# Kernel tuning notes

Hardware: AMD Instinct MI355X
Metric: run time of the kernel (lower is better)

Reference implementation:

```python
import jax, jax.numpy as jnp
import numpy as np

NCODEBOOKS, K, SUBVEC = 32, 16, 128
IN_F, OUT_F = 4096, 2048
BATCH, SEQ = 2, 1024


def setup_inputs() -> dict:
    key = jax.random.key(0)
    k1, k2, k3, k4, k5 = jax.random.split(key, 5)
    return {
        "x": jax.random.normal(k1, (BATCH, SEQ, IN_F), dtype=jnp.float32),
        "centroids": jax.random.normal(k2, (NCODEBOOKS, K, SUBVEC), dtype=jnp.float32),
        "weight": jax.random.normal(k3, (NCODEBOOKS, SUBVEC, OUT_F), dtype=jnp.float32),
        "inverse_temperature_logit": jax.random.normal(k4, (1,), dtype=jnp.float32),
        "bias": jax.random.normal(k5, (OUT_F,), dtype=jnp.float32),
    }


def reference(x, centroids, weight, inverse_temperature_logit, bias):
    shape = x.shape[:-1]
    C, k, d = centroids.shape
    # [N, C, d] -> [C, N, d]
    xr = jnp.transpose(x.reshape(-1, C, d), (1, 0, 2))
    # Euclidean cdist per codebook: [C, N, k]
    x2 = jnp.sum(xr * xr, axis=-1)[:, :, None]
    c2 = jnp.sum(centroids * centroids, axis=-1)[:, None, :]
    xc = jnp.einsum('cnd,ckd->cnk', xr, centroids)
    dist = jnp.sqrt(jnp.maximum(x2 + c2 - 2.0 * xc, 0.0))
    inv_temp = jax.nn.softplus(inverse_temperature_logit) + 1.0  # [1]
    attention = jax.nn.softmax(-dist * inv_temp, axis=-1)  # [C, N, k]
    lut = jnp.einsum('ckd,cdo->cko', centroids, weight)  # [C, k, O]
    training_output = jnp.einsum('cnk,cko->no', attention, lut)  # [N, O]
    # one-hot argmin matmul == direct gather of lut rows
    idx = jnp.argmin(dist, axis=-1)  # [C, N]
    gathered = jnp.take_along_axis(lut, idx[:, :, None], axis=1)  # [C, N, O]
    inference_output = jnp.sum(gathered, axis=0)  # [N, O]
    # straight-through estimator
    output = training_output - jax.lax.stop_gradient(training_output - inference_output)
    output = output + bias
    return output.reshape(*shape, lut.shape[-1])
```

## Files before the change

### kernel.cpp

```cpp
#include <hip/hip_runtime.h>

#define NCB 32
#define KK 16
#define DD 128
#define IN_F 4096
#define OUT_F 2048
#define NTOK 2048

__global__ __launch_bounds__(256) void lut_kernel(const float* __restrict__ centroids,
                                                  const float* __restrict__ weight,
                                                  float* __restrict__ lut,
                                                  float* __restrict__ c2out) {
    const int c = blockIdx.y;
    const int o0 = blockIdx.x * 64;
    const int lane_o = threadIdx.x & 63;
    const int dg = threadIdx.x >> 6;
    __shared__ float part[4][KK][64];

    if (blockIdx.x == 0 && threadIdx.x < KK) {
        const float* cb = centroids + ((size_t)c * KK + threadIdx.x) * DD;
        float s = 0.f;
        for (int d = 0; d < DD; ++d) { float v = cb[d]; s += v * v; }
        c2out[c * KK + threadIdx.x] = s;
    }

    float acc[KK];
#pragma unroll
    for (int k = 0; k < KK; ++k) acc[k] = 0.f;
    const float* wbase = weight + (size_t)c * DD * OUT_F + o0 + lane_o;
    const float* cbase = centroids + (size_t)c * KK * DD;
#pragma unroll
    for (int chunk = 0; chunk < 8; ++chunk) {
        const int d = dg * 32 + chunk * 4;
        float w0 = wbase[(size_t)(d + 0) * OUT_F];
        float w1 = wbase[(size_t)(d + 1) * OUT_F];
        float w2 = wbase[(size_t)(d + 2) * OUT_F];
        float w3 = wbase[(size_t)(d + 3) * OUT_F];
#pragma unroll
        for (int k = 0; k < KK; ++k) {
            float4 cv = *(const float4*)(cbase + k * DD + d);
            acc[k] += cv.x * w0 + cv.y * w1 + cv.z * w2 + cv.w * w3;
        }
    }
#pragma unroll
    for (int k = 0; k < KK; ++k) part[dg][k][lane_o] = acc[k];
    __syncthreads();
#pragma unroll
    for (int r = 0; r < 4; ++r) {
        int i = r * 256 + threadIdx.x;
        int k = i >> 6, o = i & 63;
        float s = part[0][k][o] + part[1][k][o] + part[2][k][o] + part[3][k][o];
        lut[((size_t)c * KK + k) * OUT_F + o0 + o] = s;
    }
}

__global__ __launch_bounds__(256) void idx_kernel(const float* __restrict__ x,
                                                  const float* __restrict__ centroids,
                                                  const float* __restrict__ c2,
                                                  unsigned char* __restrict__ idxb) {
    const int c = blockIdx.y;
    const int t0 = blockIdx.x * 64;
    const int tid = threadIdx.x;
    const int th_q = tid & 3;
    const int th_k = (tid >> 2) & 3;
    const int th_t = tid >> 4;

    __shared__ float cent_s[KK * 164];

    for (int p = tid; p < KK * 32; p += 256) {
        int k = p >> 5, f4 = p & 31;
        int q = f4 >> 3, jj = f4 & 7;
        *(float4*)(cent_s + k * 164 + q * 40 + jj * 4) =
            *(const float4*)(centroids + ((size_t)c * KK + k) * DD + f4 * 4);
    }
    __syncthreads();

    float c2v[4];
#pragma unroll
    for (int kk = 0; kk < 4; ++kk) c2v[kk] = c2[c * KK + th_k * 4 + kk];

    float acc[4][4];
#pragma unroll
    for (int r = 0; r < 4; ++r)
#pragma unroll
        for (int kk = 0; kk < 4; ++kk) acc[r][kk] = 0.f;

    const float* xb0 = x + (size_t)(t0 + th_t * 4) * IN_F + c * DD + th_q * 32;
#pragma unroll
    for (int chunk = 0; chunk < 8; ++chunk) {
        float4 xa[4];
#pragma unroll
        for (int r = 0; r < 4; ++r)
            xa[r] = *(const float4*)(xb0 + (size_t)r * IN_F + chunk * 4);
        float4 ca[4];
#pragma unroll
        for (int kk = 0; kk < 4; ++kk)
            ca[kk] = *(const float4*)(cent_s + (th_k * 4 + kk) * 164 + th_q * 40 + chunk * 4);
#pragma unroll
        for (int r = 0; r < 4; ++r)
#pragma unroll
            for (int kk = 0; kk < 4; ++kk)
                acc[r][kk] += xa[r].x * ca[kk].x + xa[r].y * ca[kk].y
                            + xa[r].z * ca[kk].z + xa[r].w * ca[kk].w;
    }

#pragma unroll
    for (int r = 0; r < 4; ++r)
#pragma unroll
        for (int kk = 0; kk < 4; ++kk) {
            float a = acc[r][kk];
            a += __shfl_xor(a, 1);
            a += __shfl_xor(a, 2);
            acc[r][kk] = a;
        }

#pragma unroll
    for (int r = 0; r < 4; ++r) {
        float best = c2v[0] - 2.f * acc[r][0];
        int bi = th_k * 4;
#pragma unroll
        for (int kk = 1; kk < 4; ++kk) {
            float v = c2v[kk] - 2.f * acc[r][kk];
            if (v < best) { best = v; bi = th_k * 4 + kk; }
        }
#pragma unroll
        for (int s = 4; s <= 8; s <<= 1) {
            float ov = __shfl_xor(best, s);
            int oi = __shfl_xor(bi, s);
            if (ov < best || (ov == best && oi < bi)) { best = ov; bi = oi; }
        }
        if ((tid & 15) == 0)
            idxb[(size_t)(t0 + th_t * 4 + r) * NCB + c] = (unsigned char)bi;
    }
}

__global__ __launch_bounds__(256) void gather_kernel(const float* __restrict__ lut,
                                                     const unsigned char* __restrict__ idxb,
                                                     const float* __restrict__ bias,
                                                     float* __restrict__ out) {
    const int t0 = blockIdx.x * 256;
    const int o0 = blockIdx.y * 32;
    __shared__ float slut[NCB * KK * 36];
    __shared__ unsigned char sidx[256 * NCB];

    {
        const int row = threadIdx.x >> 3;
        const int q = threadIdx.x & 7;
        for (int r = row; r < NCB * KK; r += 32)
            *(float4*)(slut + r * 36 + q * 4) =
                *(const float4*)(lut + (size_t)r * OUT_F + o0 + q * 4);
    }
    {
        const int4* ig = (const int4*)(idxb + (size_t)t0 * NCB);
        int4* is4 = (int4*)sidx;
        for (int i = threadIdx.x; i < 512; i += 256) is4[i] = ig[i];
    }
    __syncthreads();

    const int oo = (threadIdx.x & 15) * 2;
    const int tl = threadIdx.x >> 4;
    const float2 bv = *(const float2*)(bias + o0 + oo);

    for (int tt = tl; tt < 256; tt += 16) {
        float2 acc = bv;
        const unsigned int* ip = (const unsigned int*)(sidx + tt * NCB);
#pragma unroll
        for (int c4 = 0; c4 < NCB / 4; ++c4) {
            unsigned int iv4 = ip[c4];
#pragma unroll
            for (int b = 0; b < 4; ++b) {
                int cc = c4 * 4 + b;
                int iv = (iv4 >> (8 * b)) & 0xff;
                const float2 v = *(const float2*)(slut + (cc * KK + iv) * 36 + oo);
                acc.x += v.x;
                acc.y += v.y;
            }
        }
        *(float2*)(out + (size_t)(t0 + tt) * OUT_F + o0 + oo) = acc;
    }
}

extern "C" void kernel_launch(void* const* d_in, const int* in_sizes, int n_in,
                              void* d_out, int out_size, void* d_ws, size_t ws_size,
                              hipStream_t stream) {
    const float* x         = (const float*)d_in[0];
    const float* centroids = (const float*)d_in[1];
    const float* weight    = (const float*)d_in[2];
    const float* bias      = (const float*)d_in[4];
    float* out = (float*)d_out;

    float* lut = (float*)d_ws;
    unsigned char* idxb = (unsigned char*)d_ws + (4u << 20);
    float* c2 = (float*)((char*)d_ws + (4u << 20) + (64u << 10));

    lut_kernel<<<dim3(OUT_F / 64, NCB), 256, 0, stream>>>(centroids, weight, lut, c2);
    idx_kernel<<<dim3(NTOK / 64, NCB), 256, 0, stream>>>(x, centroids, c2, idxb);
    gather_kernel<<<dim3(NTOK / 256, OUT_F / 32), 256, 0, stream>>>(lut, idxb, bias, out);
}
```

Before: 163.1 us.

## Fuse LUT and index kernels into one launch with in-kernel centroid norms

Merges the LUT matmul kernel and the nearest-centroid index kernel into one launch, with block ID ranges picking the role. The index blocks now compute centroid squared norms from shared memory themselves, which removes the c2 dependency between the two former kernels. This saves one launch and lets the two independent workloads run concurrently on the GPU. The cost is extra redundant norm FLOPs in every index block and 16KB dynamic shared memory for all blocks, which may reduce occupancy.

```diff
diff --git a/kernel.cpp b/kernel.cpp
--- a/kernel.cpp
+++ b/kernel.cpp
@@ -6,131 +6,132 @@
 #define IN_F 4096
 #define OUT_F 2048
 #define NTOK 2048
+#define LUT_BLOCKS ((OUT_F / 64) * NCB)
+#define IDX_BLOCKS ((NTOK / 64) * NCB)
 
-__global__ __launch_bounds__(256) void lut_kernel(const float* __restrict__ centroids,
-                                                  const float* __restrict__ weight,
-                                                  float* __restrict__ lut,
-                                                  float* __restrict__ c2out) {
-    const int c = blockIdx.y;
-    const int o0 = blockIdx.x * 64;
-    const int lane_o = threadIdx.x & 63;
-    const int dg = threadIdx.x >> 6;
-    __shared__ float part[4][KK][64];
+__global__ __launch_bounds__(256) void fused_lut_idx(
+    const float* __restrict__ centroids, const float* __restrict__ weight,
+    const float* __restrict__ x, float* __restrict__ lut,
+    unsigned char* __restrict__ idxb) {
+    extern __shared__ float smem[];
+    const int tid = threadIdx.x;
 
-    if (blockIdx.x == 0 && threadIdx.x < KK) {
-        const float* cb = centroids + ((size_t)c * KK + threadIdx.x) * DD;
-        float s = 0.f;
-        for (int d = 0; d < DD; ++d) { float v = cb[d]; s += v * v; }
-        c2out[c * KK + threadIdx.x] = s;
-    }
+    if (blockIdx.x < LUT_BLOCKS) {
+        const int c = blockIdx.x >> 5;
+        const int o0 = (blockIdx.x & 31) * 64;
+        const int lane_o = tid & 63;
+        const int dg = tid >> 6;
+        float acc[KK];
+#pragma unroll
+        for (int k = 0; k < KK; ++k) acc[k] = 0.f;
+        const float* wbase = weight + (size_t)c * DD * OUT_F + o0 + lane_o;
+        const float* cbase = centroids + (size_t)c * KK * DD;
+#pragma unroll
+        for (int chunk = 0; chunk < 8; ++chunk) {
+            const int d = dg * 32 + chunk * 4;
+            float w0 = wbase[(size_t)(d + 0) * OUT_F];
+            float w1 = wbase[(size_t)(d + 1) * OUT_F];
+            float w2 = wbase[(size_t)(d + 2) * OUT_F];
+            float w3 = wbase[(size_t)(d + 3) * OUT_F];
+#pragma unroll
+            for (int k = 0; k < KK; ++k) {
+                float4 cv = *(const float4*)(cbase + k * DD + d);
+                acc[k] += cv.x * w0 + cv.y * w1 + cv.z * w2 + cv.w * w3;
+            }
+        }
+        float* part = smem;
+#pragma unroll
+        for (int k = 0; k < KK; ++k) part[(dg * KK + k) * 64 + lane_o] = acc[k];
+        __syncthreads();
+#pragma unroll
+        for (int r = 0; r < 4; ++r) {
+            int i = r * 256 + tid;
+            int k = i >> 6, o = i & 63;
+            float s = part[(0 * KK + k) * 64 + o] + part[(1 * KK + k) * 64 + o]
+                    + part[(2 * KK + k) * 64 + o] + part[(3 * KK + k) * 64 + o];
+            lut[((size_t)c * KK + k) * OUT_F + o0 + o] = s;
+        }
+    } else {
+        const int bid = blockIdx.x - LUT_BLOCKS;
+        const int c = bid & (NCB - 1);
+        const int t0 = (bid >> 5) * 64;
+        float* cent_s = smem;
+        const int th_q = tid & 3;
+        const int th_k = (tid >> 2) & 3;
+        const int th_t = tid >> 4;
 
-    float acc[KK];
-#pragma unroll
-    for (int k = 0; k < KK; ++k) acc[k] = 0.f;
-    const float* wbase = weight + (size_t)c * DD * OUT_F + o0 + lane_o;
-    const float* cbase = centroids + (size_t)c * KK * DD;
-#pragma unroll
-    for (int chunk = 0; chunk < 8; ++chunk) {
-        const int d = dg * 32 + chunk * 4;
-        float w0 = wbase[(size_t)(d + 0) * OUT_F];
-        float w1 = wbase[(size_t)(d + 1) * OUT_F];
-        float w2 = wbase[(size_t)(d + 2) * OUT_F];
-        float w3 = wbase[(size_t)(d + 3) * OUT_F];
-#pragma unroll
-        for (int k = 0; k < KK; ++k) {
-            float4 cv = *(const float4*)(cbase + k * DD + d);
-            acc[k] += cv.x * w0 + cv.y * w1 + cv.z * w2 + cv.w * w3;
+        for (int p = tid; p < KK * 32; p += 256) {
+            int k = p >> 5, f4 = p & 31;
+            int q = f4 >> 3, jj = f4 & 7;
+            *(float4*)(cent_s + k * 164 + q * 40 + jj * 4) =
+                *(const float4*)(centroids + ((size_t)c * KK + k) * DD + f4 * 4);
         }
-    }
-#pragma unroll
-    for (int k = 0; k < KK; ++k) part[dg][k][lane_o] = acc[k];
-    __syncthreads();
-#pragma unroll
-    for (int r = 0; r < 4; ++r) {
-        int i = r * 256 + threadIdx.x;
-        int k = i >> 6, o = i & 63;
-        float s = part[0][k][o] + part[1][k][o] + part[2][k][o] + part[3][k][o];
-        lut[((size_t)c * KK + k) * OUT_F + o0 + o] = s;
-    }
-}
+        __syncthreads();
 
-__global__ __launch_bounds__(256) void idx_kernel(const float* __restrict__ x,
-                                                  const float* __restrict__ centroids,
-                                                  const float* __restrict__ c2,
-                                                  unsigned char* __restrict__ idxb) {
-    const int c = blockIdx.y;
-    const int t0 = blockIdx.x * 64;
-    const int tid = threadIdx.x;
-    const int th_q = tid & 3;
-    const int th_k = (tid >> 2) & 3;
-    const int th_t = tid >> 4;
-
-    __shared__ float cent_s[KK * 164];
-
-    for (int p = tid; p < KK * 32; p += 256) {
-        int k = p >> 5, f4 = p & 31;
-        int q = f4 >> 3, jj = f4 & 7;
-        *(float4*)(cent_s + k * 164 + q * 40 + jj * 4) =
-            *(const float4*)(centroids + ((size_t)c * KK + k) * DD + f4 * 4);
-    }
-    __syncthreads();
-
-    float c2v[4];
-#pragma unroll
-    for (int kk = 0; kk < 4; ++kk) c2v[kk] = c2[c * KK + th_k * 4 + kk];
-
-    float acc[4][4];
-#pragma unroll
-    for (int r = 0; r < 4; ++r)
-#pragma unroll
-        for (int kk = 0; kk < 4; ++kk) acc[r][kk] = 0.f;
-
-    const float* xb0 = x + (size_t)(t0 + th_t * 4) * IN_F + c * DD + th_q * 32;
-#pragma unroll
-    for (int chunk = 0; chunk < 8; ++chunk) {
-        float4 xa[4];
-#pragma unroll
-        for (int r = 0; r < 4; ++r)
-            xa[r] = *(const float4*)(xb0 + (size_t)r * IN_F + chunk * 4);
-        float4 ca[4];
-#pragma unroll
-        for (int kk = 0; kk < 4; ++kk)
-            ca[kk] = *(const float4*)(cent_s + (th_k * 4 + kk) * 164 + th_q * 40 + chunk * 4);
+        float acc[4][4], sq[4];
 #pragma unroll
         for (int r = 0; r < 4; ++r)
 #pragma unroll
+            for (int kk = 0; kk < 4; ++kk) acc[r][kk] = 0.f;
+#pragma unroll
+        for (int kk = 0; kk < 4; ++kk) sq[kk] = 0.f;
+
+        const float* xb0 = x + (size_t)(t0 + th_t * 4) * IN_F + c * DD + th_q * 32;
+#pragma unroll
+        for (int chunk = 0; chunk < 8; ++chunk) {
+            float4 xa[4];
+#pragma unroll
+            for (int r = 0; r < 4; ++r)
+                xa[r] = *(const float4*)(xb0 + (size_t)r * IN_F + chunk * 4);
+            float4 ca[4];
+#pragma unroll
             for (int kk = 0; kk < 4; ++kk)
-                acc[r][kk] += xa[r].x * ca[kk].x + xa[r].y * ca[kk].y
-                            + xa[r].z * ca[kk].z + xa[r].w * ca[kk].w;
-    }
-
+                ca[kk] = *(const float4*)(cent_s + (th_k * 4 + kk) * 164 + th_q * 40 + chunk * 4);
 #pragma unroll
-    for (int r = 0; r < 4; ++r)
+            for (int kk = 0; kk < 4; ++kk)
+                sq[kk] += ca[kk].x * ca[kk].x + ca[kk].y * ca[kk].y
+                        + ca[kk].z * ca[kk].z + ca[kk].w * ca[kk].w;
+#pragma unroll
+            for (int r = 0; r < 4; ++r)
+#pragma unroll
+                for (int kk = 0; kk < 4; ++kk)
+                    acc[r][kk] += xa[r].x * ca[kk].x + xa[r].y * ca[kk].y
+                                + xa[r].z * ca[kk].z + xa[r].w * ca[kk].w;
+        }
 #pragma unroll
         for (int kk = 0; kk < 4; ++kk) {
-            float a = acc[r][kk];
+            float a = sq[kk];
             a += __shfl_xor(a, 1);
             a += __shfl_xor(a, 2);
-            acc[r][kk] = a;
-        }
-
-#pragma unroll
-    for (int r = 0; r < 4; ++r) {
-        float best = c2v[0] - 2.f * acc[r][0];
-        int bi = th_k * 4;
-#pragma unroll
-        for (int kk = 1; kk < 4; ++kk) {
-            float v = c2v[kk] - 2.f * acc[r][kk];
-            if (v < best) { best = v; bi = th_k * 4 + kk; }
+            sq[kk] = a;
         }
 #pragma unroll
-        for (int s = 4; s <= 8; s <<= 1) {
-            float ov = __shfl_xor(best, s);
-            int oi = __shfl_xor(bi, s);
-            if (ov < best || (ov == best && oi < bi)) { best = ov; bi = oi; }
+        for (int r = 0; r < 4; ++r)
+#pragma unroll
+            for (int kk = 0; kk < 4; ++kk) {
+                float a = acc[r][kk];
+                a += __shfl_xor(a, 1);
+                a += __shfl_xor(a, 2);
+                acc[r][kk] = a;
+            }
+#pragma unroll
+        for (int r = 0; r < 4; ++r) {
+            float best = sq[0] - 2.f * acc[r][0];
+            int bi = th_k * 4;
+#pragma unroll
+            for (int kk = 1; kk < 4; ++kk) {
+                float v = sq[kk] - 2.f * acc[r][kk];
+                if (v < best) { best = v; bi = th_k * 4 + kk; }
+            }
+#pragma unroll
+            for (int s = 4; s <= 8; s <<= 1) {
+                float ov = __shfl_xor(best, s);
+                int oi = __shfl_xor(bi, s);
+                if (ov < best || (ov == best && oi < bi)) { best = ov; bi = oi; }
+            }
+            if ((tid & 15) == 0)
+                idxb[(size_t)(t0 + th_t * 4 + r) * NCB + c] = (unsigned char)bi;
         }
-        if ((tid & 15) == 0)
-            idxb[(size_t)(t0 + th_t * 4 + r) * NCB + c] = (unsigned char)bi;
     }
 }
 
@@ -191,9 +192,8 @@
 
     float* lut = (float*)d_ws;
     unsigned char* idxb = (unsigned char*)d_ws + (4u << 20);
-    float* c2 = (float*)((char*)d_ws + (4u << 20) + (64u << 10));
 
-    lut_kernel<<<dim3(OUT_F / 64, NCB), 256, 0, stream>>>(centroids, weight, lut, c2);
-    idx_kernel<<<dim3(NTOK / 64, NCB), 256, 0, stream>>>(x, centroids, c2, idxb);
+    fused_lut_idx<<<LUT_BLOCKS + IDX_BLOCKS, 256, 16384, stream>>>(
+        centroids, weight, x, lut, idxb);
     gather_kernel<<<dim3(NTOK / 256, OUT_F / 32), 256, 0, stream>>>(lut, idxb, bias, out);
 }
```

New measurement: 160.3 us. No clear change (-1.7%).
